# Kernel optimization log

Measured on AMD Instinct MI355X. Metric: run time of the kernel, lower is better.

The kernel has to match this reference:

```python
import jax, jax.numpy as jnp
import numpy as np

BSZ, SEQ, EMBED = 2, 4096, 1024
NUM_HEADS = 16
HEAD_DIM = EMBED // NUM_HEADS
WINDOW = 256  # attention_window[layer_id]


def setup_inputs() -> dict:
    key = jax.random.key(0)
    ks = jax.random.split(key, 7)
    s = 1.0 / np.sqrt(EMBED)
    return {
        "hidden_states": jax.random.normal(ks[0], (BSZ, SEQ, EMBED), jnp.float32),
        "Wq": jax.random.normal(ks[1], (EMBED, EMBED), jnp.float32) * s,
        "bq": jnp.zeros((EMBED,), jnp.float32),
        "Wk": jax.random.normal(ks[2], (EMBED, EMBED), jnp.float32) * s,
        "bk": jnp.zeros((EMBED,), jnp.float32),
        "Wv": jax.random.normal(ks[3], (EMBED, EMBED), jnp.float32) * s,
        "bv": jnp.zeros((EMBED,), jnp.float32),
    }


def _blocks3(x, nb, w):
    # x: [b, s + 2w, h, d] -> [b, nb, 3w, h, d]; block c sees key blocks c-1, c, c+1
    b = x.shape[0]
    xb = x.reshape(b, nb + 2, w, NUM_HEADS, HEAD_DIM)
    return jnp.concatenate([xb[:, i:i + nb] for i in range(3)], axis=2)


def reference(hidden_states, Wq, bq, Wk, bk, Wv, bv):
    b, s, e = hidden_states.shape
    w = WINDOW
    nb = s // w
    q = (hidden_states @ Wq + bq) * (1.0 / np.sqrt(HEAD_DIM))
    k = hidden_states @ Wk + bk
    v = hidden_states @ Wv + bv
    q = q.reshape(b, nb, w, NUM_HEADS, HEAD_DIM)
    k = k.reshape(b, s, NUM_HEADS, HEAD_DIM)
    v = v.reshape(b, s, NUM_HEADS, HEAD_DIM)
    pad = ((0, 0), (w, w), (0, 0), (0, 0))
    kb = _blocks3(jnp.pad(k, pad), nb, w)  # [b, nb, 3w, h, d]
    vb = _blocks3(jnp.pad(v, pad), nb, w)
    # banded scores: query x in block n attends keys at global pos n*w - w + y
    scores = jnp.einsum('bnxhd,bnyhd->bnhxy', q, kb)  # [b, nb, h, w, 3w]
    x_idx = jnp.arange(w)
    y_idx = jnp.arange(3 * w)
    band = jnp.abs(y_idx[None, :] - x_idx[:, None] - w) <= w  # [w, 3w]
    kpos = jnp.arange(nb)[:, None] * w - w + y_idx[None, :]   # [nb, 3w]
    inb = (kpos >= 0) & (kpos < s)
    mask = band[None, :, :] & inb[:, None, :]                 # [nb, w, 3w]
    scores = jnp.where(mask[None, :, None, :, :], scores, -jnp.inf)
    probs = jax.nn.softmax(scores.astype(jnp.float32), axis=-1).astype(v.dtype)
    attn = jnp.einsum('bnhxy,bnyhd->bnxhd', probs, vb)        # [b, nb, w, h, d]
    return attn.reshape(b, s, e)
```

## Files before the change

kernel.cpp:

```cpp
#include <hip/hip_runtime.h>
#include <stdint.h>

#define SEQ    4096
#define EMBED  1024
#define NHEAD  16
#define HDIM   64
#define WIN    256
#define BSZ    2
#define M_TOT  (BSZ * SEQ)
#define N_QKV  3072
#define N_QK   2048
#define K_DIM  1024
#define LOG2E  1.4426950408889634f

typedef __attribute__((ext_vector_type(8))) __bf16 bf16x8;
typedef __attribute__((ext_vector_type(4))) float  f32x4;

__device__ __forceinline__ unsigned short f2bf(float f) {
  union { float f; unsigned int u; } c; c.f = f;
  unsigned int u = c.u;
  unsigned int r = (u + 0x7FFFu + ((u >> 16) & 1u)) >> 16;
  return (unsigned short)r;
}

__device__ __forceinline__ unsigned int cvt_pk_bf16(float lo, float hi) {
  unsigned int r;
  asm("v_cvt_pk_bf16_f32 %0, %1, %2" : "=v"(r) : "v"(lo), "v"(hi));
  return r;
}

__device__ __forceinline__ void gl2lds16(const void* g, void* l) {
  __builtin_amdgcn_global_load_lds((const __attribute__((address_space(1))) void*)g,
                                   (__attribute__((address_space(3))) void*)l, 16, 0, 0);
}

__global__ __launch_bounds__(256) void cvt_h(const float* __restrict__ in,
                                             unsigned short* __restrict__ out) {
  int i = (blockIdx.x * 256 + threadIdx.x) * 4;
  float4 v = *(const float4*)(in + i);
  ushort4 o;
  o.x = f2bf(v.x); o.y = f2bf(v.y); o.z = f2bf(v.z); o.w = f2bf(v.w);
  *(ushort4*)(out + i) = o;
}

__global__ __launch_bounds__(256) void cvt_w(const float* __restrict__ Wq,
                                             const float* __restrict__ Wk,
                                             const float* __restrict__ Wv,
                                             unsigned short* __restrict__ Wt) {
  __shared__ float t[32][33];
  int z = blockIdx.z;
  const float* W = (z == 0) ? Wq : (z == 1) ? Wk : Wv;
  int kb = blockIdx.x * 32, nb = blockIdx.y * 32;
  int tx = threadIdx.x, ty = threadIdx.y;
  for (int it = 0; it < 4; ++it) {
    int k = kb + ty + it * 8;
    t[ty + it * 8][tx] = W[(size_t)k * 1024 + nb + tx];
  }
  __syncthreads();
  for (int it = 0; it < 4; ++it) {
    int n = nb + ty + it * 8;
    Wt[(size_t)(z * 1024 + n) * 1024 + kb + tx] = f2bf(t[tx][ty + it * 8]);
  }
}

__global__ __launch_bounds__(256) void qkv_gemm(const unsigned short* __restrict__ A,
                                                const unsigned short* __restrict__ Bt,
                                                const float* __restrict__ bq,
                                                const float* __restrict__ bk,
                                                const float* __restrict__ bv,
                                                unsigned short* __restrict__ C,
                                                unsigned short* __restrict__ Vt) {
  __shared__ unsigned short As[128 * 64];
  __shared__ unsigned short Bs[128 * 64];
  int tid  = threadIdx.x;
  int lane = tid & 63, wave = tid >> 6;
  int ln   = lane & 15, quad = lane >> 4;
  int m0 = blockIdx.y * 128, n0 = blockIdx.x * 128;
  int wy = wave >> 1, wx = wave & 1;
  f32x4 acc[4][4];
  for (int i = 0; i < 4; ++i)
    for (int j = 0; j < 4; ++j) acc[i][j] = (f32x4){0.f, 0.f, 0.f, 0.f};

  for (int k0 = 0; k0 < K_DIM; k0 += 64) {
    __syncthreads();
    for (int it = 0; it < 4; ++it) {
      int chunk = it * 256 + wave * 64 + lane;
      int row = chunk >> 3, c = chunk & 7;
      int cg = c ^ (row & 7);
      gl2lds16(A + (size_t)(m0 + row) * K_DIM + k0 + cg * 8, As + chunk * 8);
    }
    for (int it = 0; it < 4; ++it) {
      int chunk = it * 256 + wave * 64 + lane;
      int row = chunk >> 3, c = chunk & 7;
      int cg = c ^ (row & 7);
      gl2lds16(Bt + (size_t)(n0 + row) * K_DIM + k0 + cg * 8, Bs + chunk * 8);
    }
    __syncthreads();
    for (int ks2 = 0; ks2 < 2; ++ks2) {
      bf16x8 af[4], bfr[4];
      for (int i = 0; i < 4; ++i) {
        int row = wy * 64 + i * 16 + ln;
        int c = (ks2 * 4 + quad) ^ (row & 7);
        af[i] = *(const bf16x8*)&As[row * 64 + c * 8];
      }
      for (int j = 0; j < 4; ++j) {
        int row = wx * 64 + j * 16 + ln;
        int c = (ks2 * 4 + quad) ^ (row & 7);
        bfr[j] = *(const bf16x8*)&Bs[row * 64 + c * 8];
      }
      for (int i = 0; i < 4; ++i)
        for (int j = 0; j < 4; ++j)
          acc[i][j] = __builtin_amdgcn_mfma_f32_16x16x32_bf16(af[i], bfr[j], acc[i][j], 0, 0, 0);
    }
  }

  if (n0 < N_QK) {
    for (int j = 0; j < 4; ++j) {
      int n = n0 + wx * 64 + j * 16 + ln;
      float bias, scl;
      if (n < 1024) { bias = bq[n];        scl = 0.125f * LOG2E; }
      else          { bias = bk[n - 1024]; scl = 1.f; }
      for (int i = 0; i < 4; ++i) {
        int mb = m0 + wy * 64 + i * 16 + quad * 4;
        for (int r = 0; r < 4; ++r) {
          float v = (acc[i][j][r] + bias) * scl;
          C[(size_t)(mb + r) * N_QK + n] = f2bf(v);
        }
      }
    }
  } else {
    for (int j = 0; j < 4; ++j) {
      int n  = n0 + wx * 64 + j * 16 + ln;
      int hd = n - 2048;
      float bias = bv[hd];
      for (int i = 0; i < 4; ++i) {
        int mb  = m0 + wy * 64 + i * 16 + quad * 4;
        int bb  = mb >> 12;
        int pos = mb & (SEQ - 1);
        ushort4 pk;
        pk.x = f2bf(acc[i][j][0] + bias);
        pk.y = f2bf(acc[i][j][1] + bias);
        pk.z = f2bf(acc[i][j][2] + bias);
        pk.w = f2bf(acc[i][j][3] + bias);
        *(ushort4*)&Vt[((size_t)bb * (NHEAD * HDIM) + hd) * SEQ + pos] = pk;
      }
    }
  }
}

__global__ __launch_bounds__(256) void attn(const unsigned short* __restrict__ qk,
                                            const unsigned short* __restrict__ vtg,
                                            float* __restrict__ out) {
  __shared__ unsigned short Kl[64 * 72];
  __shared__ unsigned short Vl[64 * 72];
  int tid  = threadIdx.x;
  int lane = tid & 63, wave = tid >> 6;
  int ln   = lane & 15, quad = lane >> 4;
  int bx = blockIdx.x;
  int lx = ((bx & 7) << 3) | (bx >> 3);
  int q0 = lx * 64, head = blockIdx.y, b = blockIdx.z;
  size_t baseRow = (size_t)b * SEQ;
  const unsigned short* kptr = qk + 1024;
  const unsigned short* vrow = vtg + ((size_t)(b * NHEAD + head) * HDIM) * SEQ;

  int sy = tid >> 3, sc = tid & 7;
  const unsigned short* kbase = kptr + (baseRow + sy) * (size_t)N_QK + head * HDIM + sc * 8;
  const unsigned short* vbase = vrow + (size_t)sy * SEQ + sc * 8;

  bf16x8 qf[2];
  {
    size_t ro = (baseRow + q0 + wave * 16 + ln) * (size_t)N_QK + head * HDIM + quad * 8;
    qf[0] = *(const bf16x8*)&qk[ro];
    qf[1] = *(const bf16x8*)&qk[ro + 32];
  }

  float l_st = 0.f;
  f32x4 o_acc[4];
  for (int dt = 0; dt < 4; ++dt) o_acc[dt] = (f32x4){0.f, 0.f, 0.f, 0.f};

  int lo = (q0 >= 256) ? 0 : (256 - q0) / 64;
  int hi = (SEQ + 256 - q0) / 64; if (hi > 9) hi = 9;

  uint4 pk0, pk1, pv0, pv1;
#define PREFETCH(KT)                                                        \
  {                                                                         \
    pk0 = *(const uint4*)&kbase[(size_t)(KT) * N_QK];                       \
    pk1 = *(const uint4*)&kbase[(size_t)((KT) + 32) * N_QK];                \
    pv0 = *(const uint4*)&vbase[(KT)];                                      \
    pv1 = *(const uint4*)&vbase[(size_t)32 * SEQ + (KT)];                   \
  }

  PREFETCH(q0 - 256 + lo * 64);

  int srcA = ((lane & 16) << 1) | ln;
  int srcB = srcA + 16;
  bool hiQ = (lane & 32) != 0;

  for (int t = lo; t < hi; ++t) {
    int kt = q0 - 256 + t * 64;
    __syncthreads();
    *(uint4*)&Kl[sy * 72 + sc * 8]        = pk0;
    *(uint4*)&Kl[(sy + 32) * 72 + sc * 8] = pk1;
    *(uint4*)&Vl[sy * 72 + sc * 8]        = pv0;
    *(uint4*)&Vl[(sy + 32) * 72 + sc * 8] = pv1;
    __syncthreads();

    if (t + 1 < hi) { PREFETCH(kt + 64); }

    f32x4 s[4];
    __builtin_amdgcn_s_setprio(1);
    for (int nt = 0; nt < 4; ++nt) {
      bf16x8 kf0 = *(const bf16x8*)&Kl[(nt * 16 + ln) * 72 + quad * 8];
      bf16x8 kf1 = *(const bf16x8*)&Kl[(nt * 16 + ln) * 72 + 32 + quad * 8];
      f32x4 z = (f32x4){0.f, 0.f, 0.f, 0.f};
      z = __builtin_amdgcn_mfma_f32_16x16x32_bf16(kf0, qf[0], z, 0, 0, 0);
      z = __builtin_amdgcn_mfma_f32_16x16x32_bf16(kf1, qf[1], z, 0, 0, 0);
      s[nt] = z;
    }
    __builtin_amdgcn_s_setprio(0);

    if (t == 0 || t == 8) {
      int qq = q0 + wave * 16 + ln;
      for (int nt = 0; nt < 4; ++nt) {
        int kb = kt + nt * 16 + quad * 4 - qq;
        for (int r = 0; r < 4; ++r) {
          int dd = kb + r;
          if (dd < -WIN || dd > WIN) s[nt][r] = -INFINITY;
        }
      }
    }

    float rs = 0.f;
    for (int nt = 0; nt < 4; ++nt)
      for (int r = 0; r < 4; ++r) {
        float p = exp2f(s[nt][r]);
        s[nt][r] = p;
        rs += p;
      }
    l_st += rs;

    unsigned int p01[4], p23[4];
    for (int nt = 0; nt < 4; ++nt) {
      p01[nt] = cvt_pk_bf16(s[nt][0], s[nt][1]);
      p23[nt] = cvt_pk_bf16(s[nt][2], s[nt][3]);
    }

    for (int ks = 0; ks < 2; ++ks) {
      int ntA = 2 * ks, ntB = 2 * ks + 1;
      unsigned int a0 = (unsigned int)__shfl((int)p01[ntA], srcA);
      unsigned int a1 = (unsigned int)__shfl((int)p23[ntA], srcA);
      unsigned int a2 = (unsigned int)__shfl((int)p01[ntA], srcB);
      unsigned int a3 = (unsigned int)__shfl((int)p23[ntA], srcB);
      unsigned int b0 = (unsigned int)__shfl((int)p01[ntB], srcA);
      unsigned int b1 = (unsigned int)__shfl((int)p23[ntB], srcA);
      unsigned int b2 = (unsigned int)__shfl((int)p01[ntB], srcB);
      unsigned int b3 = (unsigned int)__shfl((int)p23[ntB], srcB);
      union { uint4 u; bf16x8 v; } pf;
      pf.u.x = hiQ ? b0 : a0;
      pf.u.y = hiQ ? b1 : a1;
      pf.u.z = hiQ ? b2 : a2;
      pf.u.w = hiQ ? b3 : a3;
      __builtin_amdgcn_s_setprio(1);
      for (int dt = 0; dt < 4; ++dt) {
        bf16x8 vf = *(const bf16x8*)&Vl[(dt * 16 + ln) * 72 + ks * 32 + quad * 8];
        o_acc[dt] = __builtin_amdgcn_mfma_f32_16x16x32_bf16(vf, pf.v, o_acc[dt], 0, 0, 0);
      }
      __builtin_amdgcn_s_setprio(0);
    }
  }

  float l = l_st;
  l += __shfl_xor(l, 16);
  l += __shfl_xor(l, 32);
  float inv = 1.0f / l;
  int qpos = q0 + wave * 16 + ln;
  float* ob = out + (baseRow + qpos) * (size_t)EMBED + head * HDIM + quad * 4;
  for (int dt = 0; dt < 4; ++dt) {
    float4 v;
    v.x = o_acc[dt][0] * inv;
    v.y = o_acc[dt][1] * inv;
    v.z = o_acc[dt][2] * inv;
    v.w = o_acc[dt][3] * inv;
    *(float4*)(ob + dt * 16) = v;
  }
#undef PREFETCH
}

extern "C" void kernel_launch(void* const* d_in, const int* in_sizes, int n_in,
                              void* d_out, int out_size, void* d_ws, size_t ws_size,
                              hipStream_t stream) {
  const float* h  = (const float*)d_in[0];
  const float* Wq = (const float*)d_in[1];
  const float* bq = (const float*)d_in[2];
  const float* Wk = (const float*)d_in[3];
  const float* bk = (const float*)d_in[4];
  const float* Wv = (const float*)d_in[5];
  const float* bv = (const float*)d_in[6];
  float* out = (float*)d_out;

  unsigned short* h_bf  = (unsigned short*)d_ws;
  unsigned short* wt_bf = h_bf + (size_t)M_TOT * K_DIM;
  unsigned short* qk    = wt_bf + (size_t)N_QKV * K_DIM;
  unsigned short* vtg   = qk + (size_t)M_TOT * N_QK;

  cvt_h<<<(M_TOT * K_DIM) / 1024, 256, 0, stream>>>(h, h_bf);
  cvt_w<<<dim3(32, 32, 3), dim3(32, 8), 0, stream>>>(Wq, Wk, Wv, wt_bf);
  qkv_gemm<<<dim3(N_QKV / 128, M_TOT / 128), 256, 0, stream>>>(h_bf, wt_bf, bq, bk, bv, qk, vtg);
  attn<<<dim3(SEQ / 64, NHEAD, BSZ), 256, 0, stream>>>(qk, vtg, out);
}
```

Measured before the change: 209.9 us.

## Enlarge QKV GEMM tile to 256x256 with double-buffered LDS and block swizzle

The QKV projection GEMM moves from 128x128 tiles with 256 threads to 256x256 tiles with 512 threads. Each wave now accumulates 8x4 MFMA blocks. Global-to-LDS staging is double-buffered, so the next K slice loads while the current one is computed, and the flat block index is remapped to group neighbouring tiles for L2 reuse. MFMA sections are wrapped in s_setprio. The aim is more data reuse per LDS load and overlap of memory with compute, at the cost of 128KB of LDS per block and only 384 blocks, which can leave an uneven final wave across the CUs.

```diff
diff --git a/kernel.cpp b/kernel.cpp
--- a/kernel.cpp
+++ b/kernel.cpp
@@ -63,56 +63,73 @@
   }
 }
 
-__global__ __launch_bounds__(256) void qkv_gemm(const unsigned short* __restrict__ A,
-                                                const unsigned short* __restrict__ Bt,
-                                                const float* __restrict__ bq,
-                                                const float* __restrict__ bk,
-                                                const float* __restrict__ bv,
-                                                unsigned short* __restrict__ C,
-                                                unsigned short* __restrict__ Vt) {
-  __shared__ unsigned short As[128 * 64];
-  __shared__ unsigned short Bs[128 * 64];
+__global__ __launch_bounds__(512, 2) void qkv_gemm(const unsigned short* __restrict__ A,
+                                                   const unsigned short* __restrict__ Bt,
+                                                   const float* __restrict__ bq,
+                                                   const float* __restrict__ bk,
+                                                   const float* __restrict__ bv,
+                                                   unsigned short* __restrict__ C,
+                                                   unsigned short* __restrict__ Vt) {
+  __shared__ unsigned short As[2][256 * 64];
+  __shared__ unsigned short Bs[2][256 * 64];
   int tid  = threadIdx.x;
   int lane = tid & 63, wave = tid >> 6;
   int ln   = lane & 15, quad = lane >> 4;
-  int m0 = blockIdx.y * 128, n0 = blockIdx.x * 128;
-  int wy = wave >> 1, wx = wave & 1;
-  f32x4 acc[4][4];
-  for (int i = 0; i < 4; ++i)
+  int flat = blockIdx.y * 12 + blockIdx.x;
+  int swz  = (flat & 7) * 48 + (flat >> 3);
+  int m0 = (swz / 12) * 256, n0 = (swz % 12) * 256;
+  int wy = wave >> 2, wx = wave & 3;
+  f32x4 acc[8][4];
+  for (int i = 0; i < 8; ++i)
     for (int j = 0; j < 4; ++j) acc[i][j] = (f32x4){0.f, 0.f, 0.f, 0.f};
 
-  for (int k0 = 0; k0 < K_DIM; k0 += 64) {
-    __syncthreads();
-    for (int it = 0; it < 4; ++it) {
-      int chunk = it * 256 + wave * 64 + lane;
-      int row = chunk >> 3, c = chunk & 7;
-      int cg = c ^ (row & 7);
-      gl2lds16(A + (size_t)(m0 + row) * K_DIM + k0 + cg * 8, As + chunk * 8);
-    }
-    for (int it = 0; it < 4; ++it) {
-      int chunk = it * 256 + wave * 64 + lane;
-      int row = chunk >> 3, c = chunk & 7;
-      int cg = c ^ (row & 7);
-      gl2lds16(Bt + (size_t)(n0 + row) * K_DIM + k0 + cg * 8, Bs + chunk * 8);
-    }
-    __syncthreads();
+#define STAGE(buf, k0)                                                          \
+  do {                                                                          \
+    for (int sweep = 0; sweep < 4; ++sweep) {                                   \
+      int chunk = sweep * 512 + tid;                               \
+      int row = chunk >> 3, c = chunk & 7;                                      \
+      int cg = c ^ (row & 7);                                                   \
+      gl2lds16(A + (size_t)(m0 + row) * K_DIM + (k0) + cg * 8,                  \
+               &As[buf][chunk * 8]);                                            \
+    }                                                                           \
+    for (int sweep = 0; sweep < 4; ++sweep) {                                   \
+      int chunk = sweep * 512 + tid;                                            \
+      int row = chunk >> 3, c = chunk & 7;                                      \
+      int cg = c ^ (row & 7);                                                   \
+      gl2lds16(Bt + (size_t)(n0 + row) * K_DIM + (k0) + cg * 8,                 \
+               &Bs[buf][chunk * 8]);                                            \
+    }                                                                           \
+  } while (0)
+
+  STAGE(0, 0);
+  __syncthreads();
+
+  for (int t = 0; t < 16; ++t) {
+    int cur = t & 1;
+    if (t < 15) { STAGE(cur ^ 1, (t + 1) * 64); }
+    const unsigned short* as = As[cur];
+    const unsigned short* bs = Bs[cur];
     for (int ks2 = 0; ks2 < 2; ++ks2) {
-      bf16x8 af[4], bfr[4];
-      for (int i = 0; i < 4; ++i) {
-        int row = wy * 64 + i * 16 + ln;
+      bf16x8 af[8], bfr[4];
+      for (int i = 0; i < 8; ++i) {
+        int row = wy * 128 + i * 16 + ln;
         int c = (ks2 * 4 + quad) ^ (row & 7);
-        af[i] = *(const bf16x8*)&As[row * 64 + c * 8];
+        af[i] = *(const bf16x8*)&as[row * 64 + c * 8];
       }
       for (int j = 0; j < 4; ++j) {
         int row = wx * 64 + j * 16 + ln;
         int c = (ks2 * 4 + quad) ^ (row & 7);
-        bfr[j] = *(const bf16x8*)&Bs[row * 64 + c * 8];
-      }
-      for (int i = 0; i < 4; ++i)
+        bfr[j] = *(const bf16x8*)&bs[row * 64 + c * 8];
+      }
+      __builtin_amdgcn_s_setprio(1);
+      for (int i = 0; i < 8; ++i)
         for (int j = 0; j < 4; ++j)
           acc[i][j] = __builtin_amdgcn_mfma_f32_16x16x32_bf16(af[i], bfr[j], acc[i][j], 0, 0, 0);
-    }
-  }
+      __builtin_amdgcn_s_setprio(0);
+    }
+    __syncthreads();
+  }
+#undef STAGE
 
   if (n0 < N_QK) {
     for (int j = 0; j < 4; ++j) {
@@ -120,8 +137,8 @@
       float bias, scl;
       if (n < 1024) { bias = bq[n];        scl = 0.125f * LOG2E; }
       else          { bias = bk[n - 1024]; scl = 1.f; }
-      for (int i = 0; i < 4; ++i) {
-        int mb = m0 + wy * 64 + i * 16 + quad * 4;
+      for (int i = 0; i < 8; ++i) {
+        int mb = m0 + wy * 128 + i * 16 + quad * 4;
         for (int r = 0; r < 4; ++r) {
           float v = (acc[i][j][r] + bias) * scl;
           C[(size_t)(mb + r) * N_QK + n] = f2bf(v);
@@ -133,8 +150,8 @@
       int n  = n0 + wx * 64 + j * 16 + ln;
       int hd = n - 2048;
       float bias = bv[hd];
-      for (int i = 0; i < 4; ++i) {
-        int mb  = m0 + wy * 64 + i * 16 + quad * 4;
+      for (int i = 0; i < 8; ++i) {
+        int mb  = m0 + wy * 128 + i * 16 + quad * 4;
         int bb  = mb >> 12;
         int pos = mb & (SEQ - 1);
         ushort4 pk;
@@ -305,6 +322,6 @@
 
   cvt_h<<<(M_TOT * K_DIM) / 1024, 256, 0, stream>>>(h, h_bf);
   cvt_w<<<dim3(32, 32, 3), dim3(32, 8), 0, stream>>>(Wq, Wk, Wv, wt_bf);
-  qkv_gemm<<<dim3(N_QKV / 128, M_TOT / 128), 256, 0, stream>>>(h_bf, wt_bf, bq, bk, bv, qk, vtg);
+  qkv_gemm<<<dim3(12, 32), 512, 0, stream>>>(h_bf, wt_bf, bq, bk, bv, qk, vtg);
   attn<<<dim3(SEQ / 64, NHEAD, BSZ), 256, 0, stream>>>(qk, vtg, out);
 }
```

After: 220.7 us. 1.05x slower.
